# Performance work log

Hardware: AMD Instinct MI355X
Metric: run time of the kernel (lower is better)

The kernel has to match this reference:

```python
import jax, jax.numpy as jnp
import numpy as np

MIN_NORM = 1e-15
BALL_EPS = 4e-3  # float32 boundary eps used by the PoincareBall manifold


def _norm(x):
    return jnp.maximum(jnp.linalg.norm(x, axis=-1, keepdims=True), MIN_NORM)


def _artanh(x):
    # clamp like torch Artanh autograd fn (1e-7 margin)
    return jnp.arctanh(jnp.clip(x, -1.0 + 1e-7, 1.0 - 1e-7))


def proj(x, c):
    n = _norm(x)
    maxnorm = (1.0 - BALL_EPS) / jnp.sqrt(c)
    return jnp.where(n > maxnorm, x / n * maxnorm, x)


def expmap0(u, c):
    sc = jnp.sqrt(c)
    n = _norm(u)
    return jnp.tanh(sc * n) * u / (sc * n)


def logmap0(p, c):
    sc = jnp.sqrt(c)
    n = _norm(p)
    return _artanh(sc * n) * p / (sc * n)


def mobius_add(x, y, c):
    x2 = jnp.sum(x * x, axis=-1, keepdims=True)
    y2 = jnp.sum(y * y, axis=-1, keepdims=True)
    xy = jnp.sum(x * y, axis=-1, keepdims=True)
    num = (1.0 + 2.0 * c * xy + c * y2) * x + (1.0 - c * x2) * y
    denom = 1.0 + 2.0 * c * xy + c * c * x2 * y2
    return num / jnp.maximum(denom, MIN_NORM)


def mobius_matvec(m, x, c):
    sc = jnp.sqrt(c)
    xn = _norm(x)
    mx = x @ m.T  # [N, out]
    mxn = _norm(mx)
    res = jnp.tanh(mxn / xn * _artanh(sc * xn)) * mx / (mxn * sc)
    is_zero = jnp.all(mx == 0, axis=-1, keepdims=True)
    return jnp.where(is_zero, jnp.zeros_like(res), res)


def setup_inputs() -> dict:
    key = jax.random.key(0)
    N, D_IN, D_OUT, E = 100000, 128, 128, 1600000
    k1, k2, k3, k4, k5 = jax.random.split(key, 5)
    # points inside the Poincare ball (||x|| ~ 0.34 < 1)
    x = 0.03 * jax.random.normal(k1, (N, D_IN), dtype=jnp.float32)
    # xavier_uniform with gain sqrt(2)
    limit = np.sqrt(2.0) * np.sqrt(6.0 / (D_IN + D_OUT))
    weight = jax.random.uniform(k2, (D_OUT, D_IN), minval=-limit, maxval=limit, dtype=jnp.float32)
    bias = jnp.zeros((D_OUT,), dtype=jnp.float32)
    edge_index = jax.random.randint(k3, (2, E), 0, N, dtype=jnp.int64)
    edge_weight = jax.random.uniform(k4, (E,), dtype=jnp.float32) / 16.0
    return {"x": x, "weight": weight, "bias": bias,
            "edge_index": edge_index, "edge_weight": edge_weight,
            "num_nodes": N}


def reference(x, weight, bias, edge_index, edge_weight, num_nodes):
    c_in = 1.0
    c_out = 1.0
    # --- OriginHypLinear (dropout=0 / eval) ---
    mv = proj(mobius_matvec(weight, x, c_in), c_in)
    hyp_bias = proj(expmap0(bias[None, :], c_in), c_in)  # proj_tan0 is identity
    h = proj(mobius_add(mv, hyp_bias, c_in), c_in)
    # --- OriginHypAgg: logmap0 -> spmm -> expmap0 ---
    xt = logmap0(h, c_in)
    dst, src = edge_index[0], edge_index[1]
    support = jax.ops.segment_sum(edge_weight[:, None] * xt[src], dst,
                                  num_segments=num_nodes)
    h = proj(expmap0(support, c_in), c_in)
    # --- OriginHypAct: relu in tangent space ---
    xt = jax.nn.relu(logmap0(h, c_in))  # proj_tan0 identity
    return proj(expmap0(xt, c_out), c_out)
```

## Files before the change

kernel.cpp:

```cpp
#include <hip/hip_runtime.h>
#include <math.h>

#define D 128
#define MAXNORM 0.996f
#define MINNORM 1e-15f
#define ATCLAMP (1.0f - 1e-7f)

#define CHUNK 2048
#define BSH   7
#define MAXNB 1024
#define SCAP2 5120

typedef unsigned int   u32;
typedef unsigned short u16;

typedef __attribute__((ext_vector_type(8))) _Float16 f16x8;
typedef __attribute__((ext_vector_type(2))) __fp16   h2raw;
typedef __attribute__((ext_vector_type(4))) float f32x4;

__device__ __forceinline__ float wsum(float v) {
#pragma unroll
  for (int m = 32; m; m >>= 1) v += __shfl_xor(v, m);
  return v;
}
__device__ __forceinline__ float rsum16(float v) {
#pragma unroll
  for (int m = 1; m <= 8; m <<= 1) v += __shfl_xor(v, m);
  return v;
}

__device__ __forceinline__ float frcp(float x) { return __builtin_amdgcn_rcpf(x); }

__device__ __forceinline__ float fast_artanh(float x) {
  x = fminf(x, ATCLAMP);
  return 0.5f * __logf((1.0f + x) * frcp(1.0f - x));
}
__device__ __forceinline__ float fast_tanh(float z) {
  float t = __expf(-2.0f * z);
  return (1.0f - t) * frcp(1.0f + t);
}

__device__ __forceinline__ float bflo(u32 u) { return __uint_as_float(u << 16); }
__device__ __forceinline__ float bfhi(u32 u) { return __uint_as_float(u & 0xffff0000u); }
__device__ __forceinline__ float bf2f(u16 h) { return __uint_as_float(((u32)h) << 16); }

union H2U { h2raw h; u32 u; };
__device__ __forceinline__ u32 pkh(float a, float b) {
  H2U c; c.h = __builtin_amdgcn_cvt_pkrtz(a, b); return c.u;
}
union U2H { u32 u; _Float16 h[2]; };
union U4H8 { uint4 u; f16x8 h; };
__device__ __forceinline__ f16x8 as_h8(uint4 v) { U4H8 c; c.u = v; return c.h; }
__device__ __forceinline__ u16 f2h(float f) {
  _Float16 h = (_Float16)f; return *(u16*)&h;
}

__device__ __forceinline__ bool detect_bf16(const u32* p) {
  float lo = fabsf(bflo(p[threadIdx.x & 63]));
  return (bool)__all(lo < 1.0f);
}
__device__ __forceinline__ bool detect_i64(const int* p) {
  return (bool)__all(p[2 * (threadIdx.x & 63) + 1] == 0);
}

template<bool BF>
__device__ __forceinline__ void k1_body(const void* xv, const void* Wv,
                                        const void* bv, u16* xt, int N,
                                        uint4* Wh) {
  const int tid  = threadIdx.x;
  const int lane = tid & 63;
  const int wid  = tid >> 6;
  const int qg   = lane >> 4;
  const int lc   = lane & 15;

  for (int slot = tid; slot < 2048; slot += 256) {
    const int l = slot & 63, frag = slot >> 6;
    const int t = frag >> 2, ks = frag & 3;
    const int j  = (l & 15) + 16 * t;
    const int k0 = 32 * ks + 8 * (l >> 4);
    float f[8];
    if (BF) {
      uint4 v = ((const uint4*)Wv)[j * 16 + (k0 >> 3)];
      f[0] = bflo(v.x); f[1] = bfhi(v.x); f[2] = bflo(v.y); f[3] = bfhi(v.y);
      f[4] = bflo(v.z); f[5] = bfhi(v.z); f[6] = bflo(v.w); f[7] = bfhi(v.w);
    } else {
      const float* Wf = (const float*)Wv;
      float4 f0 = *(const float4*)(Wf + (size_t)j * D + k0);
      float4 f1 = *(const float4*)(Wf + (size_t)j * D + k0 + 4);
      f[0]=f0.x; f[1]=f0.y; f[2]=f0.z; f[3]=f0.w;
      f[4]=f1.x; f[5]=f1.y; f[6]=f1.z; f[7]=f1.w;
    }
    Wh[slot] = make_uint4(pkh(f[0],f[1]), pkh(f[2],f[3]),
                          pkh(f[4],f[5]), pkh(f[6],f[7]));
  }

  float bfr[8];
  float nb2 = 0.f;
#pragma unroll
  for (int t = 0; t < 8; ++t) {
    float v = BF ? bf2f(((const u16*)bv)[lc + 16 * t])
                 : ((const float*)bv)[lc + 16 * t];
    bfr[t] = v; nb2 += v * v;
  }
  nb2 = rsum16(nb2);
  float y2;
  {
    float nb = fmaxf(sqrtf(nb2), MINNORM);
    float s  = fast_tanh(nb) * frcp(nb);
    float n1 = s * nb;
    if (n1 > MAXNORM) s *= MAXNORM * frcp(n1);
#pragma unroll
    for (int t = 0; t < 8; ++t) bfr[t] *= s;
    y2 = s * s * nb2;
  }
  const bool bias_zero = (y2 == 0.0f);

  __syncthreads();

  const int T = (N + 15) >> 4;
  const int tile = blockIdx.x * 4 + wid;
  if (tile >= T) return;
  {
    const int rbase = tile * 16;
    int rowA = rbase + lc; if (rowA >= N) rowA = N - 1;
    uint4 Ah[4];
    float xn2 = 0.f;
#pragma unroll
    for (int ks = 0; ks < 4; ++ks) {
      float f[8];
      if (BF) {
        uint4 v = ((const uint4*)((const u16*)xv + (size_t)rowA * D))[4 * ks + qg];
        f[0]=bflo(v.x); f[1]=bfhi(v.x); f[2]=bflo(v.y); f[3]=bfhi(v.y);
        f[4]=bflo(v.z); f[5]=bfhi(v.z); f[6]=bflo(v.w); f[7]=bfhi(v.w);
      } else {
        const float4* xr = (const float4*)((const float*)xv + (size_t)rowA * D);
        float4 f0 = xr[8 * ks + 2 * qg], f1 = xr[8 * ks + 2 * qg + 1];
        f[0]=f0.x; f[1]=f0.y; f[2]=f0.z; f[3]=f0.w;
        f[4]=f1.x; f[5]=f1.y; f[6]=f1.z; f[7]=f1.w;
      }
#pragma unroll
      for (int i = 0; i < 8; ++i) xn2 += f[i] * f[i];
      Ah[ks] = make_uint4(pkh(f[0],f[1]), pkh(f[2],f[3]),
                          pkh(f[4],f[5]), pkh(f[6],f[7]));
    }
    xn2 += __shfl_xor(xn2, 16);
    xn2 += __shfl_xor(xn2, 32);

    f32x4 acc[8];
    const f32x4 zero = {0.f, 0.f, 0.f, 0.f};
#pragma unroll
    for (int t = 0; t < 8; ++t) acc[t] = zero;
#pragma unroll
    for (int ks = 0; ks < 4; ++ks) {
      f16x8 a = as_h8(Ah[ks]);
#pragma unroll
      for (int t = 0; t < 8; ++t) {
        f16x8 bh = as_h8(Wh[(t * 4 + ks) * 64 + lane]);
        acc[t] = __builtin_amdgcn_mfma_f32_16x16x32_f16(a, bh, acc[t], 0, 0, 0);
      }
    }

#pragma unroll
    for (int q = 0; q < 4; ++q) {
      const int row_off = qg * 4 + q;
      const int row = rbase + row_off;
      float xnq = fmaxf(sqrtf(__shfl(xn2, row_off)), MINNORM);
      float s2 = 0.f;
#pragma unroll
      for (int t = 0; t < 8; ++t) { float v = acc[t][q]; s2 += v * v; }
      s2 = rsum16(s2);
      float mxn = fmaxf(sqrtf(s2), MINNORM);
      float r = fast_tanh(mxn * frcp(xnq) * fast_artanh(xnq)) * frcp(mxn);
      float pn = r * mxn;
      if (pn > MAXNORM) { r *= MAXNORM * frcp(pn); pn = MAXNORM; }
      float h[8];
      float hn;
      if (bias_zero) {
#pragma unroll
        for (int t = 0; t < 8; ++t) h[t] = r * acc[t][q];
        hn = pn;
      } else {
        float xy = 0.f;
#pragma unroll
        for (int t = 0; t < 8; ++t) { h[t] = r * acc[t][q]; xy += h[t] * bfr[t]; }
        xy = rsum16(xy);
        float x2 = pn * pn;
        float ca = 1.f + 2.f * xy + y2;
        float cb = 1.f - x2;
        float id = frcp(fmaxf(1.f + 2.f * xy + x2 * y2, MINNORM));
        float s3 = 0.f;
#pragma unroll
        for (int t = 0; t < 8; ++t) { h[t] = (ca * h[t] + cb * bfr[t]) * id; s3 += h[t] * h[t]; }
        hn = fmaxf(sqrtf(rsum16(s3)), MINNORM);
      }
      float ps = (hn > MAXNORM) ? (MAXNORM * frcp(hn)) : 1.f;
      float np = fmaxf(hn * ps, MINNORM);
      float tsc = fast_artanh(np) * frcp(np) * ps;
      if (row < N) {
        uint4 pk;
        pk.x = (u32)f2h(tsc * h[0]) | ((u32)f2h(tsc * h[1]) << 16);
        pk.y = (u32)f2h(tsc * h[2]) | ((u32)f2h(tsc * h[3]) << 16);
        pk.z = (u32)f2h(tsc * h[4]) | ((u32)f2h(tsc * h[5]) << 16);
        pk.w = (u32)f2h(tsc * h[6]) | ((u32)f2h(tsc * h[7]) << 16);
        *(uint4*)(xt + (size_t)row * D + lc * 8) = pk;
      }
    }
  }
}

extern "C" __global__ __launch_bounds__(256)
void OriginHyperbolicGraphConvolution_38628935860614_kernel(
    const void* x, const void* W, const void* b, u16* xt, int* btot, int N) {
  __shared__ uint4 Wh[2048];
  if (blockIdx.x == 0)
    for (int i = threadIdx.x; i < MAXNB; i += 256) btot[i] = 0;
  if (detect_bf16((const u32*)x)) k1_body<true >(x, W, b, xt, N, Wh);
  else                            k1_body<false>(x, W, b, xt, N, Wh);
}

extern "C" __global__ __launch_bounds__(256) void ksA(
    const int* ei, const void* ew, uint2* ebuck, u16* soffs, int* btot,
    int E, int N, int nb) {
  __shared__ int   hist[MAXNB];
  __shared__ int   sArr[MAXNB + 1];
  __shared__ int   psum[256];
  __shared__ uint2 recs[CHUNK];
  const bool i64 = detect_i64(ei);
  const bool bf  = detect_bf16((const u32*)ew);
  const int tid   = threadIdx.x;
  const int cbase = blockIdx.x * CHUNK;

  for (int i = tid; i < MAXNB; i += 256) hist[i] = 0;
  __syncthreads();

  int bkt[8], rank[8]; u32 px[8], wb[8]; bool val[8];
#pragma unroll
  for (int r = 0; r < 8; ++r) {
    const int e = cbase + r * 256 + tid;
    val[r] = false;
    if (e < E) {
      int dst, src;
      if (i64) {
        dst = (int)((const uint2*)ei)[(size_t)e].x;
        src = (int)((const uint2*)ei)[(size_t)E + e].x;
      } else {
        dst = ei[e]; src = ei[(size_t)E + e];
      }
      if ((unsigned)dst < (unsigned)N && (unsigned)src < (unsigned)N) {
        val[r] = true;
        bkt[r] = dst >> BSH;
        px[r]  = (u32)src | ((u32)(dst & ((1 << BSH) - 1)) << 17);
        float w;
        if (bf) w = bf2f(((const u16*)ew)[e]); else w = ((const float*)ew)[e];
        wb[r] = __float_as_uint(w);
        rank[r] = atomicAdd(&hist[bkt[r]], 1);
      }
    }
  }
  __syncthreads();

  const int g0 = tid * 4;
  int loc[4], ts = 0;
#pragma unroll
  for (int i = 0; i < 4; ++i) { loc[i] = ts; ts += hist[g0 + i]; }
  psum[tid] = ts; __syncthreads();
#pragma unroll
  for (int off = 1; off < 256; off <<= 1) {
    int t = (tid >= off) ? psum[tid - off] : 0;
    __syncthreads();
    psum[tid] += t;
    __syncthreads();
  }
  const int excl = psum[tid] - ts;
#pragma unroll
  for (int i = 0; i < 4; ++i) sArr[g0 + i] = excl + loc[i];
  if (tid == 255) sArr[MAXNB] = psum[255];
  __syncthreads();

#pragma unroll
  for (int r = 0; r < 8; ++r) if (val[r])
    recs[sArr[bkt[r]] + rank[r]] = make_uint2(px[r], wb[r]);
  __syncthreads();

  const int vcnt = sArr[MAXNB];
  for (int i = tid; i < vcnt; i += 256) ebuck[(size_t)cbase + i] = recs[i];
  u16* so = soffs + (size_t)blockIdx.x * (nb + 1);
  for (int b = tid; b <= nb; b += 256) so[b] = (u16)sArr[b];
  for (int b = tid; b < nb; b += 256) {
    const int len = sArr[b + 1] - sArr[b];
    if (len) atomicAdd(&btot[b], len);
  }
}

extern "C" __global__ __launch_bounds__(256) void ks3(
    const uint2* ebuck, const u16* soffs, const int* btot,
    uint2* esrt, uint2* offs2, int N, int nb, int nchunks) {
  __shared__ uint2 stage[SCAP2];
  __shared__ int red[256];
  __shared__ int hist[128], sc[128], cur[128];
  __shared__ int lcur;
  const int tid = threadIdx.x;
  const int b = blockIdx.x;

  int part = 0;
  for (int i = tid; i < b; i += 256) part += btot[i];
  red[tid] = part;
  if (tid < 128) hist[tid] = 0;
  if (tid == 0) lcur = 0;
  __syncthreads();
#pragma unroll
  for (int off = 128; off; off >>= 1) {
    if (tid < off) red[tid] += red[tid + off];
    __syncthreads();
  }
  const int s0  = red[0];
  const int cnt = btot[b];
  const int node0 = b << BSH;

  const bool fit = (cnt <= SCAP2);
  if (fit) {
    for (int c = tid; c < nchunks; c += 256) {
      const u16* so = soffs + (size_t)c * (nb + 1) + b;
      const int a = so[0], e = so[1];
      if (e > a) {
        const int base = atomicAdd(&lcur, e - a);
        for (int j = a; j < e; ++j) {
          const uint2 r = ebuck[(size_t)c * CHUNK + j];
          stage[base + (j - a)] = r;
          atomicAdd(&hist[(r.x >> 17) & 127], 1);
        }
      }
    }
  } else {
    for (int c = tid; c < nchunks; c += 256) {
      const u16* so = soffs + (size_t)c * (nb + 1) + b;
      for (int j = so[0]; j < so[1]; ++j)
        atomicAdd(&hist[(ebuck[(size_t)c * CHUNK + j].x >> 17) & 127], 1);
    }
  }
  __syncthreads();

  int v = 0;
  if (tid < 128) { v = hist[tid]; sc[tid] = v; }
  __syncthreads();
#pragma unroll
  for (int off = 1; off < 128; off <<= 1) {
    int t = (tid < 128 && tid >= off) ? sc[tid - off] : 0;
    __syncthreads();
    if (tid < 128) sc[tid] += t;
    __syncthreads();
  }
  if (tid < 128) {
    const int st = sc[tid] - v;
    cur[tid] = st;
    const int node = node0 + tid;
    if (node < N) offs2[node] = make_uint2((u32)(s0 + st), (u32)v);
  }
  __syncthreads();

  if (fit) {
    for (int i = tid; i < cnt; i += 256) {
      const uint2 r = stage[i];
      const int d = atomicAdd(&cur[(r.x >> 17) & 127], 1);
      esrt[s0 + d] = make_uint2(r.x & 0x1FFFFu, r.y);
    }
  } else {
    for (int c = tid; c < nchunks; c += 256) {
      const u16* so = soffs + (size_t)c * (nb + 1) + b;
      for (int j = so[0]; j < so[1]; ++j) {
        const uint2 r = ebuck[(size_t)c * CHUNK + j];
        const int d = atomicAdd(&cur[(r.x >> 17) & 127], 1);
        esrt[s0 + d] = make_uint2(r.x & 0x1FFFFu, r.y);
      }
    }
  }
}

extern "C" __global__ __launch_bounds__(256) void kagg(
    const uint2* offs2, const uint2* esrt, const u16* xt,
    void* out, const void* xdet, int N) {
  const bool bf = detect_bf16((const u32*)xdet);
  const int lane = threadIdx.x & 63;
  const int node = blockIdx.x * 4 + (threadIdx.x >> 6);
  if (node >= N) return;
  const uint2 oo = offs2[node];
  const int s0  = __builtin_amdgcn_readfirstlane((int)oo.x);
  const int cnt = __builtin_amdgcn_readfirstlane((int)oo.y);
  const uint2* ep = esrt + s0;
  const u32* xtw = (const u32*)xt;
  float a0 = 0.f, a1 = 0.f;
  int i = 0;
  for (; i + 16 <= cnt; i += 16) {
    uint2 e[16]; u32 u[16];
#pragma unroll
    for (int k = 0; k < 16; ++k) e[k] = ep[i + k];
#pragma unroll
    for (int k = 0; k < 16; ++k) u[k] = xtw[(e[k].x << 6) | lane];
#pragma unroll
    for (int k = 0; k < 16; ++k) {
      const float w = __uint_as_float(e[k].y);
      U2H c; c.u = u[k];
      a0 += w * (float)c.h[0];
      a1 += w * (float)c.h[1];
    }
  }
  for (; i + 4 <= cnt; i += 4) {
    uint2 e[4]; u32 u[4];
#pragma unroll
    for (int k = 0; k < 4; ++k) e[k] = ep[i + k];
#pragma unroll
    for (int k = 0; k < 4; ++k) u[k] = xtw[(e[k].x << 6) | lane];
#pragma unroll
    for (int k = 0; k < 4; ++k) {
      const float w = __uint_as_float(e[k].y);
      U2H c; c.u = u[k];
      a0 += w * (float)c.h[0];
      a1 += w * (float)c.h[1];
    }
  }
  for (; i < cnt; ++i) {
    const uint2 e = ep[i];
    const u32 u = xtw[(e.x << 6) | lane];
    const float w = __uint_as_float(e.y);
    U2H c; c.u = u;
    a0 += w * (float)c.h[0];
    a1 += w * (float)c.h[1];
  }
  float n = fmaxf(sqrtf(wsum(a0 * a0 + a1 * a1)), MINNORM);
  float tn = fast_tanh(n);
  float m = tn * frcp(n);
  if (tn > MAXNORM) { m *= MAXNORM * frcp(tn); tn = MAXNORM; }
  float nn = fmaxf(tn, MINNORM);
  m *= fast_artanh(nn) * frcp(nn);
  float tA = fmaxf(m * a0, 0.f), tB = fmaxf(m * a1, 0.f);
  float nr = fmaxf(sqrtf(wsum(tA * tA + tB * tB)), MINNORM);
  float t2 = fast_tanh(nr);
  float m2 = t2 * frcp(nr);
  if (t2 > MAXNORM) m2 *= MAXNORM * frcp(t2);
  float oA = m2 * tA, oB = m2 * tB;
  const int ls = (lane & 7) * 8 + (lane >> 4);
  const int el = (lane >> 3) & 1;
  const float A0 = __shfl(oA, ls),     B0 = __shfl(oB, ls);
  const float A1 = __shfl(oA, ls + 4), B1 = __shfl(oB, ls + 4);
  const float v0 = el ? B0 : A0;
  const float v1 = el ? B1 : A1;
  if (bf) {
    u32 ua = __float_as_uint(v0), ub = __float_as_uint(v1);
    u32 ra = (ua + 0x7fffu + ((ua >> 16) & 1u)) >> 16;
    u32 rb = (ub + 0x7fffu + ((ub >> 16) & 1u)) >> 16;
    ((u32*)out)[(size_t)node * 64 + lane] = ra | (rb << 16);
  } else {
    ((float2*)out)[(size_t)node * 64 + lane] = make_float2(v0, v1);
  }
}

extern "C" void kernel_launch(void* const* d_in, const int* in_sizes, int n_in,
                              void* d_out, int out_size, void* d_ws, size_t ws_size,
                              hipStream_t stream) {
  const void* x    = d_in[0];
  const void* W    = d_in[1];
  const void* bias = d_in[2];
  const int*  ei   = (const int*)d_in[3];
  const void* ew   = d_in[4];
  const int N = in_sizes[0] / D;
  const int E = in_sizes[4];
  const int nchunks = (E + CHUNK - 1) / CHUNK;
  const int nb      = (N + (1 << BSH) - 1) >> BSH;

  char* ws = (char*)d_ws;
  size_t off = 0;
  auto carve = [&](size_t bytes) { char* p = ws + off; off = (off + bytes + 255) & ~(size_t)255; return p; };
  u16*   xt    = (u16*)  carve((size_t)N * D * sizeof(u16));
  uint2* ebuck = (uint2*)carve((size_t)nchunks * CHUNK * sizeof(uint2));
  uint2* esrt  = (uint2*)carve((size_t)E * sizeof(uint2));
  u16*   soffs = (u16*)  carve((size_t)nchunks * (nb + 1) * sizeof(u16));
  uint2* offs2 = (uint2*)carve((size_t)N * sizeof(uint2));
  int*   btot  = (int*)  carve((size_t)MAXNB * sizeof(int));

  const int T  = (N + 15) / 16;
  const int g1 = (T + 3) / 4;

  OriginHyperbolicGraphConvolution_38628935860614_kernel<<<g1, 256, 0, stream>>>(
      x, W, bias, xt, btot, N);
  ksA <<<nchunks, 256, 0, stream>>>(ei, ew, ebuck, soffs, btot, E, N, nb);
  ks3 <<<nb, 256, 0, stream>>>(ebuck, soffs, btot, esrt, offs2, N, nb, nchunks);
  kagg<<<(N + 3) / 4, 256, 0, stream>>>(offs2, esrt, xt, d_out, x, N);
}
```

Baseline: 269.3 us.

## Merge linear and edge bucketing kernels; drop global bucket-total prefix

The dense hyperbolic linear kernel and the edge-bucketing kernel become one launch, with block indices split between the two jobs so they run concurrently and one launch is saved. The global per-bucket count atomics and the serial prefix sum in ks3 are removed. Each bucket now totals its own count from the per-chunk offsets and writes into a fixed-capacity slot, or into a tail region claimed by atomic when it overflows. This trades a larger workspace and a sparser edge array for fewer launches and less serialization; the fused kernel's heavier LDS layout may affect occupancy.

```diff
diff --git a/kernel.cpp b/kernel.cpp
--- a/kernel.cpp
+++ b/kernel.cpp
@@ -10,6 +10,8 @@
 #define BSH   7
 #define MAXNB 1024
 #define SCAP2 5120
+#define CAP   4096
+#define TCAP  (1 << 20)
 
 typedef unsigned int   u32;
 typedef unsigned short u16;
@@ -208,27 +210,17 @@
   }
 }
 
-extern "C" __global__ __launch_bounds__(256)
-void OriginHyperbolicGraphConvolution_38628935860614_kernel(
-    const void* x, const void* W, const void* b, u16* xt, int* btot, int N) {
-  __shared__ uint4 Wh[2048];
-  if (blockIdx.x == 0)
-    for (int i = threadIdx.x; i < MAXNB; i += 256) btot[i] = 0;
-  if (detect_bf16((const u32*)x)) k1_body<true >(x, W, b, xt, N, Wh);
-  else                            k1_body<false>(x, W, b, xt, N, Wh);
-}
-
-extern "C" __global__ __launch_bounds__(256) void ksA(
-    const int* ei, const void* ew, uint2* ebuck, u16* soffs, int* btot,
-    int E, int N, int nb) {
-  __shared__ int   hist[MAXNB];
-  __shared__ int   sArr[MAXNB + 1];
-  __shared__ int   psum[256];
-  __shared__ uint2 recs[CHUNK];
+__device__ __forceinline__ void ksA_body(
+    const int* ei, const void* ew, uint2* ebuck, u16* soffs,
+    int E, int N, int nb, int chunk, uint4* lds) {
+  uint2* recs = (uint2*)lds;
+  int*   hist = (int*)(lds + 1024);
+  int*   sArr = hist + MAXNB;
+  int*   psum = sArr + MAXNB + 1;
   const bool i64 = detect_i64(ei);
   const bool bf  = detect_bf16((const u32*)ew);
   const int tid   = threadIdx.x;
-  const int cbase = blockIdx.x * CHUNK;
+  const int cbase = chunk * CHUNK;
 
   for (int i = tid; i < MAXNB; i += 256) hist[i] = 0;
   __syncthreads();
@@ -284,27 +276,43 @@
 
   const int vcnt = sArr[MAXNB];
   for (int i = tid; i < vcnt; i += 256) ebuck[(size_t)cbase + i] = recs[i];
-  u16* so = soffs + (size_t)blockIdx.x * (nb + 1);
+  u16* so = soffs + (size_t)chunk * (nb + 1);
   for (int b = tid; b <= nb; b += 256) so[b] = (u16)sArr[b];
-  for (int b = tid; b < nb; b += 256) {
-    const int len = sArr[b + 1] - sArr[b];
-    if (len) atomicAdd(&btot[b], len);
+}
+
+extern "C" __global__ __launch_bounds__(256)
+void OriginHyperbolicGraphConvolution_38628935860614_kernel(
+    const void* x, const void* W, const void* b, u16* xt,
+    const int* ei, const void* ew, uint2* ebuck, u16* soffs, int* tailcur,
+    int N, int E, int nb, int nk1) {
+  __shared__ uint4 Wh[2048];
+  if (blockIdx.x == 0 && threadIdx.x == 0) *tailcur = 0;
+  if ((int)blockIdx.x < nk1) {
+    if (detect_bf16((const u32*)x)) k1_body<true >(x, W, b, xt, N, Wh);
+    else                            k1_body<false>(x, W, b, xt, N, Wh);
+  } else {
+    ksA_body(ei, ew, ebuck, soffs, E, N, nb, (int)blockIdx.x - nk1, Wh);
   }
 }
 
 extern "C" __global__ __launch_bounds__(256) void ks3(
-    const uint2* ebuck, const u16* soffs, const int* btot,
-    uint2* esrt, uint2* offs2, int N, int nb, int nchunks) {
+    const uint2* ebuck, const u16* soffs, uint2* esrt, uint2* offs2,
+    int* tailcur, int N, int nb, int nchunks) {
   __shared__ uint2 stage[SCAP2];
   __shared__ int red[256];
   __shared__ int hist[128], sc[128], cur[128];
   __shared__ int lcur;
+  __shared__ u32 sbase;
   const int tid = threadIdx.x;
   const int b = blockIdx.x;
-
-  int part = 0;
-  for (int i = tid; i < b; i += 256) part += btot[i];
-  red[tid] = part;
+  const int node0 = b << BSH;
+
+  int myc = 0;
+  for (int c = tid; c < nchunks; c += 256) {
+    const u16* so = soffs + (size_t)c * (nb + 1) + b;
+    myc += (int)so[1] - (int)so[0];
+  }
+  red[tid] = myc;
   if (tid < 128) hist[tid] = 0;
   if (tid == 0) lcur = 0;
   __syncthreads();
@@ -313,9 +321,12 @@
     if (tid < off) red[tid] += red[tid + off];
     __syncthreads();
   }
-  const int s0  = red[0];
-  const int cnt = btot[b];
-  const int node0 = b << BSH;
+  const int cnt = red[0];
+  if (tid == 0)
+    sbase = (cnt <= CAP) ? (u32)((size_t)b * CAP)
+                         : (u32)((size_t)nb * CAP + (u32)atomicAdd(tailcur, cnt));
+  __syncthreads();
+  const u32 base = sbase;
 
   const bool fit = (cnt <= SCAP2);
   if (fit) {
@@ -323,10 +334,10 @@
       const u16* so = soffs + (size_t)c * (nb + 1) + b;
       const int a = so[0], e = so[1];
       if (e > a) {
-        const int base = atomicAdd(&lcur, e - a);
+        const int sb = atomicAdd(&lcur, e - a);
         for (int j = a; j < e; ++j) {
           const uint2 r = ebuck[(size_t)c * CHUNK + j];
-          stage[base + (j - a)] = r;
+          stage[sb + (j - a)] = r;
           atomicAdd(&hist[(r.x >> 17) & 127], 1);
         }
       }
@@ -354,7 +365,7 @@
     const int st = sc[tid] - v;
     cur[tid] = st;
     const int node = node0 + tid;
-    if (node < N) offs2[node] = make_uint2((u32)(s0 + st), (u32)v);
+    if (node < N) offs2[node] = make_uint2(base + (u32)st, (u32)v);
   }
   __syncthreads();
 
@@ -362,7 +373,7 @@
     for (int i = tid; i < cnt; i += 256) {
       const uint2 r = stage[i];
       const int d = atomicAdd(&cur[(r.x >> 17) & 127], 1);
-      esrt[s0 + d] = make_uint2(r.x & 0x1FFFFu, r.y);
+      esrt[(size_t)base + d] = make_uint2(r.x & 0x1FFFFu, r.y);
     }
   } else {
     for (int c = tid; c < nchunks; c += 256) {
@@ -370,7 +381,7 @@
       for (int j = so[0]; j < so[1]; ++j) {
         const uint2 r = ebuck[(size_t)c * CHUNK + j];
         const int d = atomicAdd(&cur[(r.x >> 17) & 127], 1);
-        esrt[s0 + d] = make_uint2(r.x & 0x1FFFFu, r.y);
+        esrt[(size_t)base + d] = make_uint2(r.x & 0x1FFFFu, r.y);
       }
     }
   }
@@ -472,17 +483,16 @@
   auto carve = [&](size_t bytes) { char* p = ws + off; off = (off + bytes + 255) & ~(size_t)255; return p; };
   u16*   xt    = (u16*)  carve((size_t)N * D * sizeof(u16));
   uint2* ebuck = (uint2*)carve((size_t)nchunks * CHUNK * sizeof(uint2));
-  uint2* esrt  = (uint2*)carve((size_t)E * sizeof(uint2));
+  uint2* esrt  = (uint2*)carve(((size_t)nb * CAP + TCAP) * sizeof(uint2));
   u16*   soffs = (u16*)  carve((size_t)nchunks * (nb + 1) * sizeof(u16));
   uint2* offs2 = (uint2*)carve((size_t)N * sizeof(uint2));
-  int*   btot  = (int*)  carve((size_t)MAXNB * sizeof(int));
-
-  const int T  = (N + 15) / 16;
-  const int g1 = (T + 3) / 4;
-
-  OriginHyperbolicGraphConvolution_38628935860614_kernel<<<g1, 256, 0, stream>>>(
-      x, W, bias, xt, btot, N);
-  ksA <<<nchunks, 256, 0, stream>>>(ei, ew, ebuck, soffs, btot, E, N, nb);
-  ks3 <<<nb, 256, 0, stream>>>(ebuck, soffs, btot, esrt, offs2, N, nb, nchunks);
+  int*   tailcur = (int*)carve(256);
+
+  const int T   = (N + 15) / 16;
+  const int nk1 = (T + 3) / 4;
+
+  OriginHyperbolicGraphConvolution_38628935860614_kernel<<<nk1 + nchunks, 256, 0, stream>>>(
+      x, W, bias, xt, ei, ew, ebuck, soffs, tailcur, N, E, nb, nk1);
+  ks3 <<<nb, 256, 0, stream>>>(ebuck, soffs, esrt, offs2, tailcur, N, nb, nchunks);
   kagg<<<(N + 3) / 4, 256, 0, stream>>>(offs2, esrt, xt, d_out, x, N);
 }
```

After: 253.1 us. 1.06x faster.
